# Kernel tuning notes

Measured on AMD Instinct MI355X. Metric: run time of the kernel, lower is better.

The kernel has to match this reference:

```python
import jax, jax.numpy as jnp
import numpy as np

EPS_MEAN = 1e-10


def setup_inputs() -> dict:
    key = jax.random.key(0)
    ks = jax.random.split(key, 16)
    B, N, F, D = 2, 512, 128, 3
    s = lambda fan_in: 1.0 / np.sqrt(fan_in)
    return {
        "h": jax.random.normal(ks[0], (B, N, F), jnp.float32),
        "coord": jax.random.normal(ks[1], (B, N, D), jnp.float32),
        "mask": jnp.ones((B, N), jnp.float32),
        "edge_w1": jax.random.normal(ks[2], (2 * F + 1, F), jnp.float32) * s(2 * F + 1),
        "edge_b1": jnp.zeros((F,), jnp.float32),
        "edge_w2": jax.random.normal(ks[3], (F, F), jnp.float32) * s(F),
        "edge_b2": jnp.zeros((F,), jnp.float32),
        "node_w1": jax.random.normal(ks[4], (2 * F, F), jnp.float32) * s(2 * F),
        "node_b1": jnp.zeros((F,), jnp.float32),
        "node_w2": jax.random.normal(ks[5], (F, F), jnp.float32) * s(F),
        "node_b2": jnp.zeros((F,), jnp.float32),
        "coord_w1": jax.random.normal(ks[6], (F, F), jnp.float32) * s(F),
        "coord_b1": jnp.zeros((F,), jnp.float32),
        # xavier_uniform with gain=0.001 -> tiny weights
        "coord_w2": jax.random.normal(ks[7], (F, 1), jnp.float32) * 0.001 * s(F),
    }


def reference(h, coord, mask, edge_w1, edge_b1, edge_w2, edge_b2,
              node_w1, node_b1, node_w2, node_b2,
              coord_w1, coord_b1, coord_w2):
    silu = jax.nn.silu
    B, N, F = h.shape
    # mask inputs
    h = h * mask[:, :, None]
    coord = coord * mask[:, :, None]
    mask2d = mask[:, :, None] * mask[:, None, :]            # [B,N,N]

    # coord2radial
    coord_diff = coord[:, :, None] - coord[:, None]          # [B,N,N,3]
    radial = jnp.sum(coord_diff ** 2, axis=-1, keepdims=True)  # [B,N,N,1]
    radial = radial * mask2d[..., None]
    coord_diff = coord_diff * mask2d[..., None]

    # edge model: source[b,i,j]=h[b,j], target[b,i,j]=h[b,i]
    source = jnp.broadcast_to(h[:, None, :, :], (B, N, N, F))
    target = jnp.broadcast_to(h[:, :, None, :], (B, N, N, F))
    edge_in = jnp.concatenate([source, target, radial], axis=-1)  # [B,N,N,2F+1]
    m = silu(edge_in @ edge_w1 + edge_b1)
    m = silu(m @ edge_w2 + edge_b2)                          # [B,N,N,F]
    m = m * mask2d[..., None]

    # coord model
    embed = silu(m @ coord_w1 + coord_b1) @ coord_w2         # [B,N,N,1]
    trans = coord_diff * embed * mask2d[..., None]           # [B,N,N,3]
    denom = jnp.sum(mask2d, axis=2, keepdims=True) + EPS_MEAN  # [B,N,1]
    coord_new = coord + jnp.sum(trans, axis=2) / denom
    coord_new = coord_new * mask[:, :, None]

    # node model
    agg = jnp.sum(m, axis=2)                                 # [B,N,F]
    node_in = jnp.concatenate([h, agg], axis=-1) * mask[:, :, None]
    out = silu(node_in @ node_w1 + node_b1) @ node_w2 + node_b2
    h_new = (h + out) * mask[:, :, None]

    return h_new, coord_new
```

## Files before the change

kernel.cpp:

```cpp
#include <hip/hip_runtime.h>


#define B_ 2
#define N_ 512
#define F_ 128
#define TJ 256
#define MSTRIDE 136

#define CM   (-1.44269504088896340736f)
#define INVC (-0.69314718055994530942f)

typedef __attribute__((ext_vector_type(8))) short short8;
typedef __attribute__((ext_vector_type(4))) float floatx4;
typedef __attribute__((ext_vector_type(2))) float floatx2;

#if defined(__has_builtin)
#if __has_builtin(__builtin_amdgcn_exp2f)
#define EXP2F(x) __builtin_amdgcn_exp2f(x)
#endif
#endif
#ifndef EXP2F
#define EXP2F(x) __expf((x) * 0.69314718055994530942f)
#endif

__device__ __forceinline__ float fsilu(float x) {
    float e = __expf(-x);
    return x * __builtin_amdgcn_rcpf(1.0f + e);
}
__device__ __forceinline__ floatx2 mk2(float a, float b) {
    floatx2 r; r.x = a; r.y = b; return r;
}
__device__ __forceinline__ floatx2 silu2s(floatx2 y) {
    floatx2 e;
    e.x = EXP2F(y.x);
    e.y = EXP2F(y.y);
    floatx2 d = e + 1.0f;
    floatx2 r;
    r.x = __uint_as_float(0x7EF311C3u - __float_as_uint(d.x));
    r.y = __uint_as_float(0x7EF311C3u - __float_as_uint(d.y));
    r = r * (2.0f - d * r);
    r = r * (2.0f - d * r);
    return y * r;
}
__device__ __forceinline__ unsigned cvtpk(float lo, float hi) {
    unsigned r;
    asm("v_cvt_pk_bf16_f32 %0, %1, %2" : "=v"(r) : "v"(lo), "v"(hi));
    return r;
}
__device__ __forceinline__ unsigned pack2(float a, float b) {
    return __builtin_amdgcn_perm(__float_as_uint(b) + 0x8000u,
                                 __float_as_uint(a) + 0x8000u, 0x07060302u);
}

__global__ __launch_bounds__(256) void egcl_prep(
        const float* __restrict__ h, const float* __restrict__ mask,
        const float* __restrict__ ew1, const float* __restrict__ ew2,
        const float* __restrict__ cw1,
        float* __restrict__ Hs, float* __restrict__ Ht,
        unsigned short* __restrict__ W2P, unsigned short* __restrict__ WcP,
        float* __restrict__ msum) {
    __shared__ float sh[8][F_];
    const int blk = blockIdx.x, tid = threadIdx.x;
    if (blk < 128) {
        const int r0 = blk * 8;
        const int col = tid & 127, half = tid >> 7;
#pragma unroll
        for (int rr = 0; rr < 4; ++rr) {
            int row = rr * 2 + half;
            sh[row][col] = h[(r0 + row) * F_ + col] * mask[r0 + row];
        }
        __syncthreads();
        const float* W = ew1 + half * F_ * F_ + col;
        float acc[8] = {0.f, 0.f, 0.f, 0.f, 0.f, 0.f, 0.f, 0.f};
#pragma unroll 8
        for (int k = 0; k < F_; ++k) {
            float w = W[k * F_];
#pragma unroll
            for (int r = 0; r < 8; ++r) acc[r] += sh[r][k] * w;
        }
        float* dst = half ? Ht : Hs;
#pragma unroll
        for (int r = 0; r < 8; ++r) dst[(r0 + r) * F_ + col] = acc[r] * CM;
    } else if (blk < 144) {
        const int wsel = (blk - 128) >> 3;
        const int mt = (blk - 128) & 7;
        const float* src = wsel ? cw1 : ew2;
        unsigned short* dst = wsel ? WcP : W2P;
        const int ln = tid & 63, kk = tid >> 6;
        const int qq = ln >> 4, ll = ln & 15;
#pragma unroll
        for (int rep = 0; rep < 2; ++rep) {
            const int krow = kk * 32 + qq * 8 + rep * 4;
            float f0 = src[(krow + 0) * F_ + mt * 16 + ll];
            float f1 = src[(krow + 1) * F_ + mt * 16 + ll];
            float f2 = src[(krow + 2) * F_ + mt * 16 + ll];
            float f3 = src[(krow + 3) * F_ + mt * 16 + ll];
            uint2 u = make_uint2(pack2(f0, f1), pack2(f2, f3));
            *(uint2*)(dst + ((mt * 4 + kk) * 64 + ln) * 8 + rep * 4) = u;
        }
    } else {
        const int bb = blk - 144;
        float v = mask[bb * N_ + tid] + mask[bb * N_ + 256 + tid];
        v += __shfl_xor(v, 1);  v += __shfl_xor(v, 2);
        v += __shfl_xor(v, 4);  v += __shfl_xor(v, 8);
        v += __shfl_xor(v, 16); v += __shfl_xor(v, 32);
        const int wave = tid >> 6, lane = tid & 63;
        if (lane == 0) sh[0][wave] = v;
        __syncthreads();
        if (tid == 0) msum[bb] = sh[0][0] + sh[0][1] + sh[0][2] + sh[0][3];
    }
}

#define L_W2   0
#define L_WC   32768
#define L_MS   65536
#define L_HB   135168
#define L_W1R  135680
#define L_EB2  136192
#define L_CB1  136704
#define L_CW2  137216
#define L_HIN  137728
#define L_TOTAL 138240
#define L_AGGP (L_MS + 0)
#define L_CSP  (L_MS + 4096)
#define L_NP   (L_MS + 4224)
#define L_TL   (L_MS + 6272)
#define L_AGGT (L_MS + 6784)

__global__ __launch_bounds__(512, 2) void egcl_main(
        const float* __restrict__ h, const float* __restrict__ coord,
        const float* __restrict__ mask,
        const float* __restrict__ eb1, const float* __restrict__ eb2,
        const float* __restrict__ cb1, const float* __restrict__ cw2,
        const float* __restrict__ nw1, const float* __restrict__ nb1,
        const float* __restrict__ nw2, const float* __restrict__ nb2,
        const float* __restrict__ ew1,
        const float* __restrict__ Hs, const float* __restrict__ Ht,
        const unsigned short* __restrict__ W2P,
        const unsigned short* __restrict__ WcP,
        const float* __restrict__ msum,
        float* __restrict__ out_h, float* __restrict__ out_coord) {
    extern __shared__ char smem[];
    unsigned short* W2L = (unsigned short*)(smem + L_W2);
    unsigned short* WcL = (unsigned short*)(smem + L_WC);
    unsigned short* ms  = (unsigned short*)(smem + L_MS);
    float* HB    = (float*)(smem + L_HB);
    float* W1R   = (float*)(smem + L_W1R);
    float* EB2s  = (float*)(smem + L_EB2);
    float* CB1s  = (float*)(smem + L_CB1);
    float* CW2s  = (float*)(smem + L_CW2);
    float* hin   = (float*)(smem + L_HIN);
    float* aggp  = (float*)(smem + L_AGGP);
    float* csp   = (float*)(smem + L_CSP);
    float* np    = (float*)(smem + L_NP);
    float* tl    = (float*)(smem + L_TL);
    float* aggt  = (float*)(smem + L_AGGT);

    const int tid  = threadIdx.x;
    const int wave = tid >> 6, lane = tid & 63;
    const int q = lane >> 4, l15 = lane & 15;
    const int bi = blockIdx.x;
    const int b  = bi >> 9;
    const float mask_i = mask[bi];

    {
        const uint4* s2 = (const uint4*)W2P;
        const uint4* sc = (const uint4*)WcP;
        uint4* d2 = (uint4*)(smem + L_W2);
        uint4* dc = (uint4*)(smem + L_WC);
#pragma unroll
        for (int t = 0; t < 4; ++t) {
            d2[tid + t * 512] = s2[tid + t * 512];
            dc[tid + t * 512] = sc[tid + t * 512];
        }
    }
    if (tid < F_) {
        HB[tid]   = Ht[bi * F_ + tid] + CM * eb1[tid];
        W1R[tid]  = CM * ew1[2 * F_ * F_ + tid];
        EB2s[tid] = CM * eb2[tid];
        CB1s[tid] = CM * cb1[tid];
        CW2s[tid] = INVC * cw2[tid];
        hin[tid]  = h[bi * F_ + tid] * mask_i;
    }
    const float cmi0 = coord[bi * 3 + 0] * mask_i;
    const float cmi1 = coord[bi * 3 + 1] * mask_i;
    const float cmi2 = coord[bi * 3 + 2] * mask_i;
    __syncthreads();

    const int j0 = wave * 32 + l15;
    const int j1 = j0 + 16;
    unsigned short* msr0 = ms + j0 * MSTRIDE;
    unsigned short* msr1 = ms + j1 * MSTRIDE;

    floatx2 ag2[16];
#pragma unroll
    for (int t = 0; t < 16; ++t) ag2[t] = mk2(0.f, 0.f);
    float cs0 = 0.f, cs1 = 0.f, cs2 = 0.f;

    for (int p = 0; p < N_ / TJ; ++p) {
        const int jg0 = b * N_ + p * TJ + j0;
        const int jg1 = jg0 + 16;
        const float mj0 = mask[jg0], mj1 = mask[jg1];
        const float c00 = coord[jg0 * 3 + 0] * mj0;
        const float c01 = coord[jg0 * 3 + 1] * mj0;
        const float c02 = coord[jg0 * 3 + 2] * mj0;
        const float c10 = coord[jg1 * 3 + 0] * mj1;
        const float c11 = coord[jg1 * 3 + 1] * mj1;
        const float c12 = coord[jg1 * 3 + 2] * mj1;
        const float d00 = cmi0 - c00, d01 = cmi1 - c01, d02 = cmi2 - c02;
        const float d10 = cmi0 - c10, d11 = cmi1 - c11, d12 = cmi2 - c12;
        const float f2_0 = mask_i * mj0, f2_1 = mask_i * mj1;
        const float rad0 = (d00 * d00 + d01 * d01 + d02 * d02) * f2_0;
        const float rad1 = (d10 * d10 + d11 * d11 + d12 * d12) * f2_1;
        const floatx2 rr0 = mk2(rad0, rad0), rr1 = mk2(rad1, rad1);
        const floatx2 f220 = mk2(f2_0, f2_0), f221 = mk2(f2_1, f2_1);

        short8 bfr0[4], bfr1[4];
#pragma unroll
        for (int kk = 0; kk < 4; ++kk) {
            const int ko = kk * 32 + q * 8;
            floatx4 hb0 = *(const floatx4*)(HB + ko);
            floatx4 hb1 = *(const floatx4*)(HB + ko + 4);
            floatx4 w10 = *(const floatx4*)(W1R + ko);
            floatx4 w11 = *(const floatx4*)(W1R + ko + 4);
            {
                floatx4 hsA = *(const floatx4*)(Hs + jg0 * F_ + ko);
                floatx4 hsB = *(const floatx4*)(Hs + jg0 * F_ + ko + 4);
                floatx2 y0 = mk2(hsA[0], hsA[1]) + mk2(hb0[0], hb0[1]) + rr0 * mk2(w10[0], w10[1]);
                floatx2 y1 = mk2(hsA[2], hsA[3]) + mk2(hb0[2], hb0[3]) + rr0 * mk2(w10[2], w10[3]);
                floatx2 y2 = mk2(hsB[0], hsB[1]) + mk2(hb1[0], hb1[1]) + rr0 * mk2(w11[0], w11[1]);
                floatx2 y3 = mk2(hsB[2], hsB[3]) + mk2(hb1[2], hb1[3]) + rr0 * mk2(w11[2], w11[3]);
                floatx2 x0 = silu2s(y0), x1 = silu2s(y1);
                floatx2 x2 = silu2s(y2), x3 = silu2s(y3);
                union { short8 s8; unsigned u[4]; } pu;
                pu.u[0] = cvtpk(x0.x, x0.y); pu.u[1] = cvtpk(x1.x, x1.y);
                pu.u[2] = cvtpk(x2.x, x2.y); pu.u[3] = cvtpk(x3.x, x3.y);
                bfr0[kk] = pu.s8;
            }
            {
                floatx4 hsA = *(const floatx4*)(Hs + jg1 * F_ + ko);
                floatx4 hsB = *(const floatx4*)(Hs + jg1 * F_ + ko + 4);
                floatx2 y0 = mk2(hsA[0], hsA[1]) + mk2(hb0[0], hb0[1]) + rr1 * mk2(w10[0], w10[1]);
                floatx2 y1 = mk2(hsA[2], hsA[3]) + mk2(hb0[2], hb0[3]) + rr1 * mk2(w10[2], w10[3]);
                floatx2 y2 = mk2(hsB[0], hsB[1]) + mk2(hb1[0], hb1[1]) + rr1 * mk2(w11[0], w11[1]);
                floatx2 y3 = mk2(hsB[2], hsB[3]) + mk2(hb1[2], hb1[3]) + rr1 * mk2(w11[2], w11[3]);
                floatx2 x0 = silu2s(y0), x1 = silu2s(y1);
                floatx2 x2 = silu2s(y2), x3 = silu2s(y3);
                union { short8 s8; unsigned u[4]; } pu;
                pu.u[0] = cvtpk(x0.x, x0.y); pu.u[1] = cvtpk(x1.x, x1.y);
                pu.u[2] = cvtpk(x2.x, x2.y); pu.u[3] = cvtpk(x3.x, x3.y);
                bfr1[kk] = pu.s8;
            }
        }

#pragma unroll
        for (int s = 0; s < 8; ++s) {
            floatx4 bias = *(const floatx4*)(EB2s + s * 16 + q * 4);
            floatx4 a0 = bias, a1 = bias;
#pragma unroll
            for (int kk = 0; kk < 4; ++kk) {
                short8 wf = *(const short8*)(W2L + ((s * 4 + kk) * 64 + lane) * 8);
                a0 = __builtin_amdgcn_mfma_f32_16x16x32_bf16(wf, bfr0[kk], a0, 0, 0, 0);
                a1 = __builtin_amdgcn_mfma_f32_16x16x32_bf16(wf, bfr1[kk], a1, 0, 0, 0);
            }
            floatx2 p00 = silu2s(mk2(a0[0], a0[1])) * f220;
            floatx2 p01 = silu2s(mk2(a0[2], a0[3])) * f220;
            floatx2 p10 = silu2s(mk2(a1[0], a1[1])) * f221;
            floatx2 p11 = silu2s(mk2(a1[2], a1[3])) * f221;
            ag2[2 * s]     += p00 + p10;
            ag2[2 * s + 1] += p01 + p11;
            *(uint2*)(msr0 + s * 16 + q * 4) =
                make_uint2(cvtpk(p00.x, p00.y), cvtpk(p01.x, p01.y));
            *(uint2*)(msr1 + s * 16 + q * 4) =
                make_uint2(cvtpk(p10.x, p10.y), cvtpk(p11.x, p11.y));
        }

        short8 mfr0[4], mfr1[4];
#pragma unroll
        for (int kk = 0; kk < 4; ++kk) {
            mfr0[kk] = *(const short8*)(msr0 + kk * 32 + q * 8);
            mfr1[kk] = *(const short8*)(msr1 + kk * 32 + q * 8);
        }
        floatx2 esv0 = mk2(0.f, 0.f), esv1 = mk2(0.f, 0.f);
#pragma unroll
        for (int s = 0; s < 8; ++s) {
            floatx4 cb = *(const floatx4*)(CB1s + s * 16 + q * 4);
            floatx4 a0 = cb, a1 = cb;
#pragma unroll
            for (int kk = 0; kk < 4; ++kk) {
                short8 wf = *(const short8*)(WcL + ((s * 4 + kk) * 64 + lane) * 8);
                a0 = __builtin_amdgcn_mfma_f32_16x16x32_bf16(wf, mfr0[kk], a0, 0, 0, 0);
                a1 = __builtin_amdgcn_mfma_f32_16x16x32_bf16(wf, mfr1[kk], a1, 0, 0, 0);
            }
            floatx4 wv = *(const floatx4*)(CW2s + s * 16 + q * 4);
            esv0 += silu2s(mk2(a0[0], a0[1])) * mk2(wv[0], wv[1]);
            esv0 += silu2s(mk2(a0[2], a0[3])) * mk2(wv[2], wv[3]);
            esv1 += silu2s(mk2(a1[0], a1[1])) * mk2(wv[0], wv[1]);
            esv1 += silu2s(mk2(a1[2], a1[3])) * mk2(wv[2], wv[3]);
        }
        float es0 = esv0.x + esv0.y;
        float es1 = esv1.x + esv1.y;
        es0 += __shfl_xor(es0, 16); es0 += __shfl_xor(es0, 32);
        es1 += __shfl_xor(es1, 16); es1 += __shfl_xor(es1, 32);
        if (q == 0) {
            float w0 = es0 * f2_0 * f2_0;
            float w1 = es1 * f2_1 * f2_1;
            cs0 += d00 * w0 + d10 * w1;
            cs1 += d01 * w0 + d11 * w1;
            cs2 += d02 * w0 + d12 * w1;
        }
    }

#pragma unroll
    for (int t = 0; t < 16; ++t) {
        float vx = ag2[t].x, vy = ag2[t].y;
        vx += __shfl_xor(vx, 1); vx += __shfl_xor(vx, 2);
        vx += __shfl_xor(vx, 4); vx += __shfl_xor(vx, 8);
        vy += __shfl_xor(vy, 1); vy += __shfl_xor(vy, 2);
        vy += __shfl_xor(vy, 4); vy += __shfl_xor(vy, 8);
        ag2[t] = mk2(vx, vy);
    }
    cs0 += __shfl_xor(cs0, 1); cs0 += __shfl_xor(cs0, 2);
    cs0 += __shfl_xor(cs0, 4); cs0 += __shfl_xor(cs0, 8);
    cs1 += __shfl_xor(cs1, 1); cs1 += __shfl_xor(cs1, 2);
    cs1 += __shfl_xor(cs1, 4); cs1 += __shfl_xor(cs1, 8);
    cs2 += __shfl_xor(cs2, 1); cs2 += __shfl_xor(cs2, 2);
    cs2 += __shfl_xor(cs2, 4); cs2 += __shfl_xor(cs2, 8);

    __syncthreads();
    if (l15 == 0) {
#pragma unroll
        for (int s = 0; s < 8; ++s) {
            floatx4 o = {ag2[2 * s].x, ag2[2 * s].y,
                         ag2[2 * s + 1].x, ag2[2 * s + 1].y};
            *(floatx4*)(aggp + wave * F_ + s * 16 + q * 4) = o;
        }
    }
    if (lane == 0) {
        csp[wave * 3 + 0] = cs0;
        csp[wave * 3 + 1] = cs1;
        csp[wave * 3 + 2] = cs2;
    }
    __syncthreads();
    if (tid < F_) {
        float s = 0.f;
#pragma unroll
        for (int w = 0; w < 8; ++w) s += aggp[w * F_ + tid];
        aggt[tid] = s * (mask_i * INVC);
    }
    __syncthreads();
    {
        const int col = tid & 127, q2 = tid >> 7;
        const int half = q2 & 1, kh = q2 >> 1;
        const float* W = nw1 + (half * 128 + kh * 64) * F_ + col;
        const float* src = half ? (aggt + kh * 64) : (hin + kh * 64);
        float s = 0.f;
#pragma unroll 8
        for (int k = 0; k < 64; ++k) s += src[k] * W[k * F_];
        if (half == 0) s *= mask_i;
        np[tid] = s;
    }
    __syncthreads();
    if (tid < F_)
        tl[tid] = fsilu(np[tid] + np[128 + tid] + np[256 + tid] +
                        np[384 + tid] + nb1[tid]);
    __syncthreads();
    if (tid < F_) {
        float s = nb2[tid];
#pragma unroll 8
        for (int k = 0; k < F_; ++k) s += tl[k] * nw2[k * F_ + tid];
        out_h[bi * F_ + tid] = (hin[tid] + s) * mask_i;
    } else if (tid < F_ + 3) {
        int d = tid - F_;
        float denom = mask_i * msum[b] + 1e-10f;
        float cm = (d == 0) ? cmi0 : ((d == 1) ? cmi1 : cmi2);
        float cst = 0.f;
#pragma unroll
        for (int w = 0; w < 8; ++w) cst += csp[w * 3 + d];
        out_coord[bi * 3 + d] = (cm + cst * __builtin_amdgcn_rcpf(denom)) * mask_i;
    }
}

extern "C" void kernel_launch(void* const* d_in, const int* in_sizes, int n_in,
                              void* d_out, int out_size, void* d_ws, size_t ws_size,
                              hipStream_t stream) {
    const float* h     = (const float*)d_in[0];
    const float* coord = (const float*)d_in[1];
    const float* mask  = (const float*)d_in[2];
    const float* ew1   = (const float*)d_in[3];
    const float* eb1   = (const float*)d_in[4];
    const float* ew2   = (const float*)d_in[5];
    const float* eb2   = (const float*)d_in[6];
    const float* nw1   = (const float*)d_in[7];
    const float* nb1   = (const float*)d_in[8];
    const float* nw2   = (const float*)d_in[9];
    const float* nb2   = (const float*)d_in[10];
    const float* cw1   = (const float*)d_in[11];
    const float* cb1   = (const float*)d_in[12];
    const float* cw2   = (const float*)d_in[13];

    float* Hs = (float*)d_ws;
    float* Ht = Hs + B_ * N_ * F_;
    unsigned short* W2P = (unsigned short*)(Ht + B_ * N_ * F_);
    unsigned short* WcP = W2P + F_ * F_;
    float* msum = (float*)(WcP + F_ * F_);

    float* out_h = (float*)d_out;
    float* out_coord = out_h + B_ * N_ * F_;

    static int attr_done = 0;
    if (!attr_done) {
        (void)hipFuncSetAttribute((const void*)egcl_main,
                                  hipFuncAttributeMaxDynamicSharedMemorySize,
                                  L_TOTAL);
        attr_done = 1;
    }

    egcl_prep<<<146, 256, 0, stream>>>(h, mask, ew1, ew2, cw1,
                                       Hs, Ht, W2P, WcP, msum);
    egcl_main<<<B_ * N_, 512, L_TOTAL, stream>>>(
        h, coord, mask, eb1, eb2, cb1, cw2, nw1, nb1, nw2, nb2, ew1,
        Hs, Ht, W2P, WcP, msum, out_h, out_coord);
}
```

Measured before the change: 193.6 us.

## Halve block size and read packed weights from global instead of LDS

```diff
diff --git a/kernel.cpp b/kernel.cpp
--- a/kernel.cpp
+++ b/kernel.cpp
@@ -4,7 +4,7 @@
 #define B_ 2
 #define N_ 512
 #define F_ 128
-#define TJ 256
+#define TJ 128
 #define MSTRIDE 136
 
 #define CM   (-1.44269504088896340736f)
@@ -111,23 +111,21 @@
     }
 }
 
-#define L_W2   0
-#define L_WC   32768
-#define L_MS   65536
-#define L_HB   135168
-#define L_W1R  135680
-#define L_EB2  136192
-#define L_CB1  136704
-#define L_CW2  137216
-#define L_HIN  137728
-#define L_TOTAL 138240
+#define L_MS   0
+#define L_HB   34816
+#define L_W1R  35328
+#define L_EB2  35840
+#define L_CB1  36352
+#define L_CW2  36864
+#define L_HIN  37376
+#define L_TOTAL 37888
 #define L_AGGP (L_MS + 0)
-#define L_CSP  (L_MS + 4096)
-#define L_NP   (L_MS + 4224)
-#define L_TL   (L_MS + 6272)
-#define L_AGGT (L_MS + 6784)
-
-__global__ __launch_bounds__(512, 2) void egcl_main(
+#define L_CSP  (L_MS + 2048)
+#define L_NP   (L_MS + 2112)
+#define L_TL   (L_MS + 3136)
+#define L_AGGT (L_MS + 3648)
+
+__global__ __launch_bounds__(256, 2) void egcl_main(
         const float* __restrict__ h, const float* __restrict__ coord,
         const float* __restrict__ mask,
         const float* __restrict__ eb1, const float* __restrict__ eb2,
@@ -141,8 +139,6 @@
         const float* __restrict__ msum,
         float* __restrict__ out_h, float* __restrict__ out_coord) {
     extern __shared__ char smem[];
-    unsigned short* W2L = (unsigned short*)(smem + L_W2);
-    unsigned short* WcL = (unsigned short*)(smem + L_WC);
     unsigned short* ms  = (unsigned short*)(smem + L_MS);
     float* HB    = (float*)(smem + L_HB);
     float* W1R   = (float*)(smem + L_W1R);
@@ -163,17 +159,6 @@
     const int b  = bi >> 9;
     const float mask_i = mask[bi];
 
-    {
-        const uint4* s2 = (const uint4*)W2P;
-        const uint4* sc = (const uint4*)WcP;
-        uint4* d2 = (uint4*)(smem + L_W2);
-        uint4* dc = (uint4*)(smem + L_WC);
-#pragma unroll
-        for (int t = 0; t < 4; ++t) {
-            d2[tid + t * 512] = s2[tid + t * 512];
-            dc[tid + t * 512] = sc[tid + t * 512];
-        }
-    }
     if (tid < F_) {
         HB[tid]   = Ht[bi * F_ + tid] + CM * eb1[tid];
         W1R[tid]  = CM * ew1[2 * F_ * F_ + tid];
@@ -259,7 +244,7 @@
             floatx4 a0 = bias, a1 = bias;
 #pragma unroll
             for (int kk = 0; kk < 4; ++kk) {
-                short8 wf = *(const short8*)(W2L + ((s * 4 + kk) * 64 + lane) * 8);
+                short8 wf = *(const short8*)(W2P + ((s * 4 + kk) * 64 + lane) * 8);
                 a0 = __builtin_amdgcn_mfma_f32_16x16x32_bf16(wf, bfr0[kk], a0, 0, 0, 0);
                 a1 = __builtin_amdgcn_mfma_f32_16x16x32_bf16(wf, bfr1[kk], a1, 0, 0, 0);
             }
@@ -288,7 +273,7 @@
             floatx4 a0 = cb, a1 = cb;
 #pragma unroll
             for (int kk = 0; kk < 4; ++kk) {
-                short8 wf = *(const short8*)(WcL + ((s * 4 + kk) * 64 + lane) * 8);
+                short8 wf = *(const short8*)(WcP + ((s * 4 + kk) * 64 + lane) * 8);
                 a0 = __builtin_amdgcn_mfma_f32_16x16x32_bf16(wf, mfr0[kk], a0, 0, 0, 0);
                 a1 = __builtin_amdgcn_mfma_f32_16x16x32_bf16(wf, mfr1[kk], a1, 0, 0, 0);
             }
@@ -342,28 +327,26 @@
         csp[wave * 3 + 2] = cs2;
     }
     __syncthreads();
-    if (tid < F_) {
+    if (tid < F_)
+        aggt[tid] = (aggp[tid] + aggp[F_ + tid] + aggp[2 * F_ + tid] +
+                     aggp[3 * F_ + tid]) * (mask_i * INVC);
+    __syncthreads();
+    {
+        int half = tid >> 7, col = tid & 127;
+        const float* W = nw1 + half * 128 * F_ + col;
         float s = 0.f;
-#pragma unroll
-        for (int w = 0; w < 8; ++w) s += aggp[w * F_ + tid];
-        aggt[tid] = s * (mask_i * INVC);
-    }
-    __syncthreads();
-    {
-        const int col = tid & 127, q2 = tid >> 7;
-        const int half = q2 & 1, kh = q2 >> 1;
-        const float* W = nw1 + (half * 128 + kh * 64) * F_ + col;
-        const float* src = half ? (aggt + kh * 64) : (hin + kh * 64);
-        float s = 0.f;
+        if (half == 0) {
 #pragma unroll 8
-        for (int k = 0; k < 64; ++k) s += src[k] * W[k * F_];
-        if (half == 0) s *= mask_i;
+            for (int k = 0; k < F_; ++k) s += hin[k] * W[k * F_];
+            s *= mask_i;
+        } else {
+#pragma unroll 8
+            for (int k = 0; k < F_; ++k) s += aggt[k] * W[k * F_];
+        }
         np[tid] = s;
     }
     __syncthreads();
-    if (tid < F_)
-        tl[tid] = fsilu(np[tid] + np[128 + tid] + np[256 + tid] +
-                        np[384 + tid] + nb1[tid]);
+    if (tid < F_) tl[tid] = fsilu(np[tid] + np[128 + tid] + nb1[tid]);
     __syncthreads();
     if (tid < F_) {
         float s = nb2[tid];
@@ -374,9 +357,7 @@
         int d = tid - F_;
         float denom = mask_i * msum[b] + 1e-10f;
         float cm = (d == 0) ? cmi0 : ((d == 1) ? cmi1 : cmi2);
-        float cst = 0.f;
-#pragma unroll
-        for (int w = 0; w < 8; ++w) cst += csp[w * 3 + d];
+        float cst = csp[d] + csp[3 + d] + csp[6 + d] + csp[9 + d];
         out_coord[bi * 3 + d] = (cm + cst * __builtin_amdgcn_rcpf(denom)) * mask_i;
     }
 }
@@ -408,17 +389,9 @@
     float* out_h = (float*)d_out;
     float* out_coord = out_h + B_ * N_ * F_;
 
-    static int attr_done = 0;
-    if (!attr_done) {
-        (void)hipFuncSetAttribute((const void*)egcl_main,
-                                  hipFuncAttributeMaxDynamicSharedMemorySize,
-                                  L_TOTAL);
-        attr_done = 1;
-    }
-
     egcl_prep<<<146, 256, 0, stream>>>(h, mask, ew1, ew2, cw1,
                                        Hs, Ht, W2P, WcP, msum);
-    egcl_main<<<B_ * N_, 512, L_TOTAL, stream>>>(
+    egcl_main<<<B_ * N_, 256, L_TOTAL, stream>>>(
         h, coord, mask, eb1, eb2, cb1, cw2, nw1, nb1, nw2, nb2, ew1,
         Hs, Ht, W2P, WcP, msum, out_h, out_coord);
 }
```

New measurement: 244.4 us. +26.2%, slower.

## Keep coord-MLP weights in registers per wave and shrink edge tile to one j per lane

Applied to the files above, without the earlier changes.

```diff
diff --git a/kernel.cpp b/kernel.cpp
--- a/kernel.cpp
+++ b/kernel.cpp
@@ -4,8 +4,8 @@
 #define B_ 2
 #define N_ 512
 #define F_ 128
-#define TJ 256
-#define MSTRIDE 136
+#define TJ 128
+#define MSTRIDE 144
 
 #define CM   (-1.44269504088896340736f)
 #define INVC (-0.69314718055994530942f)
@@ -112,15 +112,13 @@
 }
 
 #define L_W2   0
-#define L_WC   32768
-#define L_MS   65536
-#define L_HB   135168
-#define L_W1R  135680
-#define L_EB2  136192
-#define L_CB1  136704
-#define L_CW2  137216
-#define L_HIN  137728
-#define L_TOTAL 138240
+#define L_MS   32768
+#define L_EMBP 69632
+#define L_HB   73728
+#define L_W1R  74240
+#define L_EB2  74752
+#define L_HIN  75264
+#define L_TOTAL 75776
 #define L_AGGP (L_MS + 0)
 #define L_CSP  (L_MS + 4096)
 #define L_NP   (L_MS + 4224)
@@ -142,13 +140,11 @@
         float* __restrict__ out_h, float* __restrict__ out_coord) {
     extern __shared__ char smem[];
     unsigned short* W2L = (unsigned short*)(smem + L_W2);
-    unsigned short* WcL = (unsigned short*)(smem + L_WC);
     unsigned short* ms  = (unsigned short*)(smem + L_MS);
+    float* embp  = (float*)(smem + L_EMBP);
     float* HB    = (float*)(smem + L_HB);
     float* W1R   = (float*)(smem + L_W1R);
     float* EB2s  = (float*)(smem + L_EB2);
-    float* CB1s  = (float*)(smem + L_CB1);
-    float* CW2s  = (float*)(smem + L_CW2);
     float* hin   = (float*)(smem + L_HIN);
     float* aggp  = (float*)(smem + L_AGGP);
     float* csp   = (float*)(smem + L_CSP);
@@ -165,32 +161,35 @@
 
     {
         const uint4* s2 = (const uint4*)W2P;
-        const uint4* sc = (const uint4*)WcP;
         uint4* d2 = (uint4*)(smem + L_W2);
-        uint4* dc = (uint4*)(smem + L_WC);
-#pragma unroll
-        for (int t = 0; t < 4; ++t) {
-            d2[tid + t * 512] = s2[tid + t * 512];
-            dc[tid + t * 512] = sc[tid + t * 512];
-        }
+#pragma unroll
+        for (int t = 0; t < 4; ++t) d2[tid + t * 512] = s2[tid + t * 512];
     }
     if (tid < F_) {
         HB[tid]   = Ht[bi * F_ + tid] + CM * eb1[tid];
         W1R[tid]  = CM * ew1[2 * F_ * F_ + tid];
         EB2s[tid] = CM * eb2[tid];
-        CB1s[tid] = CM * cb1[tid];
-        CW2s[tid] = INVC * cw2[tid];
         hin[tid]  = h[bi * F_ + tid] * mask_i;
     }
     const float cmi0 = coord[bi * 3 + 0] * mask_i;
     const float cmi1 = coord[bi * 3 + 1] * mask_i;
     const float cmi2 = coord[bi * 3 + 2] * mask_i;
-    __syncthreads();
-
-    const int j0 = wave * 32 + l15;
-    const int j1 = j0 + 16;
-    unsigned short* msr0 = ms + j0 * MSTRIDE;
-    unsigned short* msr1 = ms + j1 * MSTRIDE;
+
+    short8 wcf[4];
+#pragma unroll
+    for (int kk = 0; kk < 4; ++kk)
+        wcf[kk] = *(const short8*)(WcP + ((wave * 4 + kk) * 64 + lane) * 8);
+    const floatx4 c1b = (*(const floatx4*)(cb1 + wave * 16 + q * 4)) * CM;
+    floatx2 w2c2[2];
+    {
+        floatx4 wv = *(const floatx4*)(cw2 + wave * 16 + q * 4);
+        w2c2[0] = mk2(wv[0], wv[1]) * INVC;
+        w2c2[1] = mk2(wv[2], wv[3]) * INVC;
+    }
+    __syncthreads();
+
+    const int jl = wave * 16 + l15;
+    unsigned short* msr = ms + jl * MSTRIDE;
 
     floatx2 ag2[16];
 #pragma unroll
@@ -198,24 +197,18 @@
     float cs0 = 0.f, cs1 = 0.f, cs2 = 0.f;
 
     for (int p = 0; p < N_ / TJ; ++p) {
-        const int jg0 = b * N_ + p * TJ + j0;
-        const int jg1 = jg0 + 16;
-        const float mj0 = mask[jg0], mj1 = mask[jg1];
-        const float c00 = coord[jg0 * 3 + 0] * mj0;
-        const float c01 = coord[jg0 * 3 + 1] * mj0;
-        const float c02 = coord[jg0 * 3 + 2] * mj0;
-        const float c10 = coord[jg1 * 3 + 0] * mj1;
-        const float c11 = coord[jg1 * 3 + 1] * mj1;
-        const float c12 = coord[jg1 * 3 + 2] * mj1;
-        const float d00 = cmi0 - c00, d01 = cmi1 - c01, d02 = cmi2 - c02;
-        const float d10 = cmi0 - c10, d11 = cmi1 - c11, d12 = cmi2 - c12;
-        const float f2_0 = mask_i * mj0, f2_1 = mask_i * mj1;
-        const float rad0 = (d00 * d00 + d01 * d01 + d02 * d02) * f2_0;
-        const float rad1 = (d10 * d10 + d11 * d11 + d12 * d12) * f2_1;
-        const floatx2 rr0 = mk2(rad0, rad0), rr1 = mk2(rad1, rad1);
-        const floatx2 f220 = mk2(f2_0, f2_0), f221 = mk2(f2_1, f2_1);
-
-        short8 bfr0[4], bfr1[4];
+        const int jg = b * N_ + p * TJ + jl;
+        const float mj = mask[jg];
+        const float c0 = coord[jg * 3 + 0] * mj;
+        const float c1 = coord[jg * 3 + 1] * mj;
+        const float c2 = coord[jg * 3 + 2] * mj;
+        const float d0 = cmi0 - c0, d1 = cmi1 - c1, d2 = cmi2 - c2;
+        const float f2 = mask_i * mj;
+        const float rad = (d0 * d0 + d1 * d1 + d2 * d2) * f2;
+        const floatx2 rr = mk2(rad, rad);
+        const floatx2 f22 = mk2(f2, f2);
+
+        short8 bfr[4];
 #pragma unroll
         for (int kk = 0; kk < 4; ++kk) {
             const int ko = kk * 32 + q * 8;
@@ -223,91 +216,63 @@
             floatx4 hb1 = *(const floatx4*)(HB + ko + 4);
             floatx4 w10 = *(const floatx4*)(W1R + ko);
             floatx4 w11 = *(const floatx4*)(W1R + ko + 4);
-            {
-                floatx4 hsA = *(const floatx4*)(Hs + jg0 * F_ + ko);
-                floatx4 hsB = *(const floatx4*)(Hs + jg0 * F_ + ko + 4);
-                floatx2 y0 = mk2(hsA[0], hsA[1]) + mk2(hb0[0], hb0[1]) + rr0 * mk2(w10[0], w10[1]);
-                floatx2 y1 = mk2(hsA[2], hsA[3]) + mk2(hb0[2], hb0[3]) + rr0 * mk2(w10[2], w10[3]);
-                floatx2 y2 = mk2(hsB[0], hsB[1]) + mk2(hb1[0], hb1[1]) + rr0 * mk2(w11[0], w11[1]);
-                floatx2 y3 = mk2(hsB[2], hsB[3]) + mk2(hb1[2], hb1[3]) + rr0 * mk2(w11[2], w11[3]);
-                floatx2 x0 = silu2s(y0), x1 = silu2s(y1);
-                floatx2 x2 = silu2s(y2), x3 = silu2s(y3);
-                union { short8 s8; unsigned u[4]; } pu;
-                pu.u[0] = cvtpk(x0.x, x0.y); pu.u[1] = cvtpk(x1.x, x1.y);
-                pu.u[2] = cvtpk(x2.x, x2.y); pu.u[3] = cvtpk(x3.x, x3.y);
-                bfr0[kk] = pu.s8;
-            }
-            {
-                floatx4 hsA = *(const floatx4*)(Hs + jg1 * F_ + ko);
-                floatx4 hsB = *(const floatx4*)(Hs + jg1 * F_ + ko + 4);
-                floatx2 y0 = mk2(hsA[0], hsA[1]) + mk2(hb0[0], hb0[1]) + rr1 * mk2(w10[0], w10[1]);
-                floatx2 y1 = mk2(hsA[2], hsA[3]) + mk2(hb0[2], hb0[3]) + rr1 * mk2(w10[2], w10[3]);
-                floatx2 y2 = mk2(hsB[0], hsB[1]) + mk2(hb1[0], hb1[1]) + rr1 * mk2(w11[0], w11[1]);
-                floatx2 y3 = mk2(hsB[2], hsB[3]) + mk2(hb1[2], hb1[3]) + rr1 * mk2(w11[2], w11[3]);
-                floatx2 x0 = silu2s(y0), x1 = silu2s(y1);
-                floatx2 x2 = silu2s(y2), x3 = silu2s(y3);
-                union { short8 s8; unsigned u[4]; } pu;
-                pu.u[0] = cvtpk(x0.x, x0.y); pu.u[1] = cvtpk(x1.x, x1.y);
-                pu.u[2] = cvtpk(x2.x, x2.y); pu.u[3] = cvtpk(x3.x, x3.y);
-                bfr1[kk] = pu.s8;
-            }
+            floatx4 hsA = *(const floatx4*)(Hs + jg * F_ + ko);
+            floatx4 hsB = *(const floatx4*)(Hs + jg * F_ + ko + 4);
+            floatx2 y0 = mk2(hsA[0], hsA[1]) + mk2(hb0[0], hb0[1]) + rr * mk2(w10[0], w10[1]);
+            floatx2 y1 = mk2(hsA[2], hsA[3]) + mk2(hb0[2], hb0[3]) + rr * mk2(w10[2], w10[3]);
+            floatx2 y2 = mk2(hsB[0], hsB[1]) + mk2(hb1[0], hb1[1]) + rr * mk2(w11[0], w11[1]);
+            floatx2 y3 = mk2(hsB[2], hsB[3]) + mk2(hb1[2], hb1[3]) + rr * mk2(w11[2], w11[3]);
+            floatx2 x0 = silu2s(y0), x1 = silu2s(y1);
+            floatx2 x2 = silu2s(y2), x3 = silu2s(y3);
+            union { short8 s8; unsigned u[4]; } pu;
+            pu.u[0] = cvtpk(x0.x, x0.y); pu.u[1] = cvtpk(x1.x, x1.y);
+            pu.u[2] = cvtpk(x2.x, x2.y); pu.u[3] = cvtpk(x3.x, x3.y);
+            bfr[kk] = pu.s8;
         }
 
 #pragma unroll
         for (int s = 0; s < 8; ++s) {
-            floatx4 bias = *(const floatx4*)(EB2s + s * 16 + q * 4);
-            floatx4 a0 = bias, a1 = bias;
+            floatx4 a = *(const floatx4*)(EB2s + s * 16 + q * 4);
 #pragma unroll
             for (int kk = 0; kk < 4; ++kk) {
                 short8 wf = *(const short8*)(W2L + ((s * 4 + kk) * 64 + lane) * 8);
-                a0 = __builtin_amdgcn_mfma_f32_16x16x32_bf16(wf, bfr0[kk], a0, 0, 0, 0);
-                a1 = __builtin_amdgcn_mfma_f32_16x16x32_bf16(wf, bfr1[kk], a1, 0, 0, 0);
+                a = __builtin_amdgcn_mfma_f32_16x16x32_bf16(wf, bfr[kk], a, 0, 0, 0);
             }
-            floatx2 p00 = silu2s(mk2(a0[0], a0[1])) * f220;
-            floatx2 p01 = silu2s(mk2(a0[2], a0[3])) * f220;
-            floatx2 p10 = silu2s(mk2(a1[0], a1[1])) * f221;
-            floatx2 p11 = silu2s(mk2(a1[2], a1[3])) * f221;
-            ag2[2 * s]     += p00 + p10;
-            ag2[2 * s + 1] += p01 + p11;
-            *(uint2*)(msr0 + s * 16 + q * 4) =
-                make_uint2(cvtpk(p00.x, p00.y), cvtpk(p01.x, p01.y));
-            *(uint2*)(msr1 + s * 16 + q * 4) =
-                make_uint2(cvtpk(p10.x, p10.y), cvtpk(p11.x, p11.y));
-        }
-
-        short8 mfr0[4], mfr1[4];
-#pragma unroll
-        for (int kk = 0; kk < 4; ++kk) {
-            mfr0[kk] = *(const short8*)(msr0 + kk * 32 + q * 8);
-            mfr1[kk] = *(const short8*)(msr1 + kk * 32 + q * 8);
-        }
-        floatx2 esv0 = mk2(0.f, 0.f), esv1 = mk2(0.f, 0.f);
-#pragma unroll
-        for (int s = 0; s < 8; ++s) {
-            floatx4 cb = *(const floatx4*)(CB1s + s * 16 + q * 4);
-            floatx4 a0 = cb, a1 = cb;
+            floatx2 p0 = silu2s(mk2(a[0], a[1])) * f22;
+            floatx2 p1 = silu2s(mk2(a[2], a[3])) * f22;
+            ag2[2 * s]     += p0;
+            ag2[2 * s + 1] += p1;
+            *(uint2*)(msr + s * 16 + q * 4) =
+                make_uint2(cvtpk(p0.x, p0.y), cvtpk(p1.x, p1.y));
+        }
+        __syncthreads();
+
+#pragma unroll
+        for (int jt = 0; jt < 8; ++jt) {
+            const unsigned short* mr = ms + (jt * 16 + l15) * MSTRIDE;
+            floatx4 a = c1b;
 #pragma unroll
             for (int kk = 0; kk < 4; ++kk) {
-                short8 wf = *(const short8*)(WcL + ((s * 4 + kk) * 64 + lane) * 8);
-                a0 = __builtin_amdgcn_mfma_f32_16x16x32_bf16(wf, mfr0[kk], a0, 0, 0, 0);
-                a1 = __builtin_amdgcn_mfma_f32_16x16x32_bf16(wf, mfr1[kk], a1, 0, 0, 0);
+                short8 bf = *(const short8*)(mr + kk * 32 + q * 8);
+                a = __builtin_amdgcn_mfma_f32_16x16x32_bf16(wcf[kk], bf, a, 0, 0, 0);
             }
-            floatx4 wv = *(const floatx4*)(CW2s + s * 16 + q * 4);
-            esv0 += silu2s(mk2(a0[0], a0[1])) * mk2(wv[0], wv[1]);
-            esv0 += silu2s(mk2(a0[2], a0[3])) * mk2(wv[2], wv[3]);
-            esv1 += silu2s(mk2(a1[0], a1[1])) * mk2(wv[0], wv[1]);
-            esv1 += silu2s(mk2(a1[2], a1[3])) * mk2(wv[2], wv[3]);
-        }
-        float es0 = esv0.x + esv0.y;
-        float es1 = esv1.x + esv1.y;
-        es0 += __shfl_xor(es0, 16); es0 += __shfl_xor(es0, 32);
-        es1 += __shfl_xor(es1, 16); es1 += __shfl_xor(es1, 32);
+            floatx2 esv = silu2s(mk2(a[0], a[1])) * w2c2[0] +
+                          silu2s(mk2(a[2], a[3])) * w2c2[1];
+            float es = esv.x + esv.y;
+            es += __shfl_xor(es, 16);
+            es += __shfl_xor(es, 32);
+            if (q == 0) embp[wave * F_ + jt * 16 + l15] = es;
+        }
+        __syncthreads();
+
         if (q == 0) {
-            float w0 = es0 * f2_0 * f2_0;
-            float w1 = es1 * f2_1 * f2_1;
-            cs0 += d00 * w0 + d10 * w1;
-            cs1 += d01 * w0 + d11 * w1;
-            cs2 += d02 * w0 + d12 * w1;
+            float e = 0.f;
+#pragma unroll
+            for (int wf = 0; wf < 8; ++wf) e += embp[wf * F_ + jl];
+            float w = e * f2 * f2;
+            cs0 += d0 * w;
+            cs1 += d1 * w;
+            cs2 += d2 * w;
         }
     }
 
```

Measured after the change: 216.2 us. 11.7% more time.
